# Optimization experiments

Measured on AMD Instinct MI355X. Metric: run time of the kernel, lower is better.

Reference implementation:

```python
import jax, jax.numpy as jnp
import numpy as np


def setup_inputs() -> dict:
    key = jax.random.key(0)
    x = jax.random.normal(key, (64, 512, 16, 16), dtype=jnp.float32)
    return {"x": x}


def reference(x):
    # x: [B, dim, h, w] -> covariance pooling y: [B, dim, dim]
    B, dim, h, w = x.shape
    M = h * w
    xf = x.reshape(B, dim, M)
    # I_hat = (1/M) I - (1/M^2) 11^T  (centering matrix scaled by 1/M)
    inv_M = jnp.asarray(1.0 / M, dtype=x.dtype)
    I_hat = inv_M * jnp.eye(M, dtype=x.dtype) - (inv_M * inv_M) * jnp.ones((M, M), dtype=x.dtype)
    # y = x @ I_hat @ x^T, I_hat broadcast over batch
    xI = jnp.einsum('bdm,mn->bdn', xf, I_hat)   # [B, dim, M]
    y = jnp.einsum('bdn,ben->bde', xI, xf)      # [B, dim, dim]
    return y
```

## Files before the change

kernel.cpp:

```cpp
#include <hip/hip_runtime.h>
#include <stdint.h>


typedef __attribute__((ext_vector_type(8))) short bf16x8;
typedef __attribute__((ext_vector_type(4))) float f32x4;

static __device__ __forceinline__ unsigned short f2bf(float f) {
    union { float f; uint32_t u; } c; c.f = f;
    uint32_t u = c.u;
    return (unsigned short)((u + 0x7FFFu + ((u >> 16) & 1u)) >> 16);
}

static __device__ __forceinline__ void cvt_store(f32x4 v0, f32x4 v1, float* psum,
                                                 unsigned short* dst) {
    *psum += (v0.x + v0.y + v0.z + v0.w) + (v1.x + v1.y + v1.z + v1.w);
    bf16x8 o;
    o[0] = (short)f2bf(v0.x); o[1] = (short)f2bf(v0.y);
    o[2] = (short)f2bf(v0.z); o[3] = (short)f2bf(v0.w);
    o[4] = (short)f2bf(v1.x); o[5] = (short)f2bf(v1.y);
    o[6] = (short)f2bf(v1.z); o[7] = (short)f2bf(v1.w);
    *(bf16x8*)dst = o;
}

static __device__ __forceinline__ void bar_lds() {
    asm volatile("s_waitcnt lgkmcnt(0)" ::: "memory");
    __builtin_amdgcn_s_barrier();
    asm volatile("" ::: "memory");
}

__global__ __launch_bounds__(256, 2) void covpool_fused(const float* __restrict__ x,
                                                        float* __restrict__ y) {
    __shared__ __align__(16) float shf[128 * 132];
    __shared__ float muA[128];
    __shared__ float muB[128];
    unsigned short* const Sbase = (unsigned short*)shf;

    const int xcd = blockIdx.x & 7;
    const int j   = blockIdx.x >> 3;
    const int b   = xcd * 8 + j / 10;
    const int t10 = j % 10;
    const unsigned code = (unsigned)((0xFBA7653210ULL >> (4 * t10)) & 15ULL);
    const int tm = code >> 2, tn = code & 3;
    const bool diag = (tm == tn);

    const float* Ag = x + ((size_t)b * 512 + tm * 128) * 256;
    const float* Bg = x + ((size_t)b * 512 + tn * 128) * 256;

    const int tid  = threadIdx.x;
    const int lane = tid & 63;
    const int wave = tid >> 6;
    const int wm = (wave >> 1) * 64;
    const int wn = (wave & 1) * 64;

    f32x4 acc[4][4] = {};
    float pA[2] = {0.f, 0.f}, pB[2] = {0.f, 0.f};

    const int rl  = lane & 15;
    const int q   = lane >> 4;
    const int swl = (q ^ ((rl >> 1) & 3)) * 8;
    const int srow = tid >> 2, schunk = tid & 3;
    const int slot = schunk ^ ((srow >> 1) & 3);

    f32x4 a0[2], a1[2], b0[2], b1[2];
#pragma unroll
    for (int t = 0; t < 2; ++t) {
        const float* g = Ag + (size_t)(t * 64 + srow) * 256 + schunk * 8;
        a0[t] = *(const f32x4*)g; a1[t] = *(const f32x4*)(g + 4);
        if (!diag) {
            const float* h = Bg + (size_t)(t * 64 + srow) * 256 + schunk * 8;
            b0[t] = *(const f32x4*)h; b1[t] = *(const f32x4*)(h + 4);
        }
    }
#pragma unroll
    for (int t = 0; t < 2; ++t) {
        const int row = t * 64 + srow;
        cvt_store(a0[t], a1[t], &pA[t], Sbase + row * 32 + slot * 8);
        if (!diag) cvt_store(b0[t], b1[t], &pB[t], Sbase + 8192 + row * 32 + slot * 8);
    }
#pragma unroll
    for (int t = 0; t < 2; ++t) {
        const float* g = Ag + (size_t)(t * 64 + srow) * 256 + 32 + schunk * 8;
        a0[t] = *(const f32x4*)g; a1[t] = *(const f32x4*)(g + 4);
        if (!diag) {
            const float* h = Bg + (size_t)(t * 64 + srow) * 256 + 32 + schunk * 8;
            b0[t] = *(const f32x4*)h; b1[t] = *(const f32x4*)(h + 4);
        }
    }
    bar_lds();

#pragma unroll
    for (int kk = 0; kk < 8; ++kk) {
        const unsigned short* Acur = Sbase + (kk & 1) * 4096;
        const unsigned short* Bcur = diag ? Acur : (Sbase + 8192 + (kk & 1) * 4096);
        bf16x8 af[4], bfr[4];
#pragma unroll
        for (int i = 0; i < 4; ++i)
            af[i] = *(const bf16x8*)(Acur + (wm + i * 16 + rl) * 32 + swl);
#pragma unroll
        for (int jj = 0; jj < 4; ++jj)
            bfr[jj] = *(const bf16x8*)(Bcur + (wn + jj * 16 + rl) * 32 + swl);
#pragma unroll
        for (int i = 0; i < 4; ++i)
#pragma unroll
            for (int jj = 0; jj < 4; ++jj)
                acc[i][jj] = __builtin_amdgcn_mfma_f32_16x16x32_bf16(
                    af[i], bfr[jj], acc[i][jj], 0, 0, 0);
        if (kk < 7) {
            const int nb = (kk + 1) & 1;
#pragma unroll
            for (int t = 0; t < 2; ++t) {
                const int row = t * 64 + srow;
                cvt_store(a0[t], a1[t], &pA[t], Sbase + nb * 4096 + row * 32 + slot * 8);
                if (!diag) cvt_store(b0[t], b1[t], &pB[t],
                                     Sbase + 8192 + nb * 4096 + row * 32 + slot * 8);
            }
            if (kk < 6) {
#pragma unroll
                for (int t = 0; t < 2; ++t) {
                    const float* g = Ag + (size_t)(t * 64 + srow) * 256 + (kk + 2) * 32 + schunk * 8;
                    a0[t] = *(const f32x4*)g; a1[t] = *(const f32x4*)(g + 4);
                    if (!diag) {
                        const float* h = Bg + (size_t)(t * 64 + srow) * 256 + (kk + 2) * 32 + schunk * 8;
                        b0[t] = *(const f32x4*)h; b1[t] = *(const f32x4*)(h + 4);
                    }
                }
            }
            bar_lds();
        }
    }

#pragma unroll
    for (int t = 0; t < 2; ++t) {
        float s = pA[t];
        s += __shfl_xor(s, 1, 64); s += __shfl_xor(s, 2, 64);
        if (schunk == 0) muA[t * 64 + srow] = s * (1.0f / 256.0f);
        if (!diag) {
            float sb = pB[t];
            sb += __shfl_xor(sb, 1, 64); sb += __shfl_xor(sb, 2, 64);
            if (schunk == 0) muB[t * 64 + srow] = sb * (1.0f / 256.0f);
        }
    }
    bar_lds();

    const float* muBp = diag ? muA : muB;
    float* yb = y + (size_t)b * 512 * 512;
    const float inv256 = 1.0f / 256.0f;

#pragma unroll
    for (int i = 0; i < 4; ++i)
#pragma unroll
        for (int jj = 0; jj < 4; ++jj) {
            const int col = wn + jj * 16 + rl;
            const float mb = muBp[col];
#pragma unroll
            for (int r = 0; r < 4; ++r) {
                const int row = wm + i * 16 + q * 4 + r;
                shf[row * 132 + col] = acc[i][jj][r] * inv256 - muA[row] * mb;
            }
        }
    bar_lds();

#pragma unroll
    for (int v = 0; v < 16; ++v) {
        const int flat = v * 256 + tid;
        const int rloc = flat >> 5, c4 = flat & 31;
        f32x4 val = *(const f32x4*)(shf + rloc * 132 + c4 * 4);
        __builtin_nontemporal_store(
            val, (f32x4*)(yb + (size_t)(tm * 128 + rloc) * 512 + tn * 128 + c4 * 4));
    }
    if (!diag) {
#pragma unroll
        for (int v = 0; v < 16; ++v) {
            const int id   = v * 256 + tid;
            const int cseg = id >> 10;
            const int cc   = (id >> 3) & 127;
            const int g    = id & 7;
            f32x4 val;
#pragma unroll
            for (int e = 0; e < 4; ++e)
                val[e] = shf[(cseg * 32 + g * 4 + e) * 132 + cc];
            __builtin_nontemporal_store(
                val, (f32x4*)(yb + (size_t)(tn * 128 + cc) * 512 + tm * 128 + cseg * 32 + g * 4));
        }
    }
}

extern "C" void kernel_launch(void* const* d_in, const int* in_sizes, int n_in,
                              void* d_out, int out_size, void* d_ws, size_t ws_size,
                              hipStream_t stream) {
    const float* x = (const float*)d_in[0];
    float* yout = (float*)d_out;
    (void)d_ws; (void)ws_size;
    covpool_fused<<<640, 256, 0, stream>>>(x, yout);
}
```

Measured before the change: 107.6 us.

## Shrink LDS by staging epilogue in 32-row chunks to raise occupancy

Replaces the 128x132 float epilogue staging buffer with a 32 KB bf16 buffer that is reused as a 32x132 float staging area. The epilogue now runs in four chunks: the owning waves write 32 rows, then all threads store them, with barriers between chunks. The launch-bounds occupancy hint is also dropped. The smaller LDS footprint lets more blocks share a CU, in exchange for extra barriers and serialized writeout.

```diff
diff --git a/kernel.cpp b/kernel.cpp
--- a/kernel.cpp
+++ b/kernel.cpp
@@ -28,12 +28,12 @@
     asm volatile("" ::: "memory");
 }
 
-__global__ __launch_bounds__(256, 2) void covpool_fused(const float* __restrict__ x,
-                                                        float* __restrict__ y) {
-    __shared__ __align__(16) float shf[128 * 132];
+__global__ __launch_bounds__(256) void covpool_fused(const float* __restrict__ x,
+                                                     float* __restrict__ y) {
+    __shared__ __align__(16) unsigned short SU[16384];
     __shared__ float muA[128];
     __shared__ float muB[128];
-    unsigned short* const Sbase = (unsigned short*)shf;
+    float* const Ep = (float*)SU;
 
     const int xcd = blockIdx.x & 7;
     const int j   = blockIdx.x >> 3;
@@ -74,8 +74,8 @@
 #pragma unroll
     for (int t = 0; t < 2; ++t) {
         const int row = t * 64 + srow;
-        cvt_store(a0[t], a1[t], &pA[t], Sbase + row * 32 + slot * 8);
-        if (!diag) cvt_store(b0[t], b1[t], &pB[t], Sbase + 8192 + row * 32 + slot * 8);
+        cvt_store(a0[t], a1[t], &pA[t], SU + row * 32 + slot * 8);
+        if (!diag) cvt_store(b0[t], b1[t], &pB[t], SU + 4096 + row * 32 + slot * 8);
     }
 #pragma unroll
     for (int t = 0; t < 2; ++t) {
@@ -90,8 +90,8 @@
 
 #pragma unroll
     for (int kk = 0; kk < 8; ++kk) {
-        const unsigned short* Acur = Sbase + (kk & 1) * 4096;
-        const unsigned short* Bcur = diag ? Acur : (Sbase + 8192 + (kk & 1) * 4096);
+        const unsigned short* Acur = SU + (kk & 1) * 8192;
+        const unsigned short* Bcur = diag ? Acur : (Acur + 4096);
         bf16x8 af[4], bfr[4];
 #pragma unroll
         for (int i = 0; i < 4; ++i)
@@ -106,13 +106,13 @@
                 acc[i][jj] = __builtin_amdgcn_mfma_f32_16x16x32_bf16(
                     af[i], bfr[jj], acc[i][jj], 0, 0, 0);
         if (kk < 7) {
-            const int nb = (kk + 1) & 1;
+            const int nb = ((kk + 1) & 1) * 8192;
 #pragma unroll
             for (int t = 0; t < 2; ++t) {
                 const int row = t * 64 + srow;
-                cvt_store(a0[t], a1[t], &pA[t], Sbase + nb * 4096 + row * 32 + slot * 8);
+                cvt_store(a0[t], a1[t], &pA[t], SU + nb + row * 32 + slot * 8);
                 if (!diag) cvt_store(b0[t], b1[t], &pB[t],
-                                     Sbase + 8192 + nb * 4096 + row * 32 + slot * 8);
+                                     SU + nb + 4096 + row * 32 + slot * 8);
             }
             if (kk < 6) {
 #pragma unroll
@@ -140,47 +140,52 @@
             if (schunk == 0) muB[t * 64 + srow] = sb * (1.0f / 256.0f);
         }
     }
-    bar_lds();
-
     const float* muBp = diag ? muA : muB;
     float* yb = y + (size_t)b * 512 * 512;
     const float inv256 = 1.0f / 256.0f;
 
 #pragma unroll
-    for (int i = 0; i < 4; ++i)
-#pragma unroll
-        for (int jj = 0; jj < 4; ++jj) {
-            const int col = wn + jj * 16 + rl;
-            const float mb = muBp[col];
-#pragma unroll
-            for (int r = 0; r < 4; ++r) {
-                const int row = wm + i * 16 + q * 4 + r;
-                shf[row * 132 + col] = acc[i][jj][r] * inv256 - muA[row] * mb;
-            }
-        }
-    bar_lds();
-
-#pragma unroll
-    for (int v = 0; v < 16; ++v) {
-        const int flat = v * 256 + tid;
-        const int rloc = flat >> 5, c4 = flat & 31;
-        f32x4 val = *(const f32x4*)(shf + rloc * 132 + c4 * 4);
-        __builtin_nontemporal_store(
-            val, (f32x4*)(yb + (size_t)(tm * 128 + rloc) * 512 + tn * 128 + c4 * 4));
-    }
-    if (!diag) {
-#pragma unroll
-        for (int v = 0; v < 16; ++v) {
-            const int id   = v * 256 + tid;
-            const int cseg = id >> 10;
-            const int cc   = (id >> 3) & 127;
-            const int g    = id & 7;
-            f32x4 val;
-#pragma unroll
-            for (int e = 0; e < 4; ++e)
-                val[e] = shf[(cseg * 32 + g * 4 + e) * 132 + cc];
+    for (int c = 0; c < 4; ++c) {
+        bar_lds();
+        if ((wave >> 1) == (c >> 1)) {
+            const int ii0 = 2 * (c & 1);
+#pragma unroll
+            for (int ii = 0; ii < 2; ++ii) {
+                const int i = ii0 + ii;
+#pragma unroll
+                for (int jj = 0; jj < 4; ++jj) {
+                    const int col = wn + jj * 16 + rl;
+                    const float mb = muBp[col];
+#pragma unroll
+                    for (int r = 0; r < 4; ++r) {
+                        const int row = wm + i * 16 + q * 4 + r;
+                        Ep[(ii * 16 + q * 4 + r) * 132 + col] =
+                            acc[i][jj][r] * inv256 - muA[row] * mb;
+                    }
+                }
+            }
+        }
+        bar_lds();
+#pragma unroll
+        for (int v = 0; v < 4; ++v) {
+            const int flat = v * 256 + tid;
+            const int rloc = flat >> 5, c4 = flat & 31;
+            f32x4 val = *(const f32x4*)(Ep + rloc * 132 + c4 * 4);
             __builtin_nontemporal_store(
-                val, (f32x4*)(yb + (size_t)(tn * 128 + cc) * 512 + tm * 128 + cseg * 32 + g * 4));
+                val, (f32x4*)(yb + (size_t)(tm * 128 + c * 32 + rloc) * 512 + tn * 128 + c4 * 4));
+        }
+        if (!diag) {
+#pragma unroll
+            for (int v = 0; v < 4; ++v) {
+                const int id = v * 256 + tid;
+                const int cc = id >> 3, g = id & 7;
+                f32x4 val;
+#pragma unroll
+                for (int e = 0; e < 4; ++e)
+                    val[e] = Ep[(g * 4 + e) * 132 + cc];
+                __builtin_nontemporal_store(
+                    val, (f32x4*)(yb + (size_t)(tn * 128 + cc) * 512 + tm * 128 + c * 32 + g * 4));
+            }
         }
     }
 }
@@ -190,6 +195,6 @@
                               hipStream_t stream) {
     const float* x = (const float*)d_in[0];
     float* yout = (float*)d_out;
-    (void)d_ws; (void)ws_size;
+    (void)d_ws; (void)ws_size; (void)in_sizes; (void)n_in; (void)out_size;
     covpool_fused<<<640, 256, 0, stream>>>(x, yout);
 }
```

Result: slower. 118.9 us (+10.5%).
